# Kernel optimization log

Measured on AMD Instinct MI355X. Metric: run time of the kernel, lower is better.

Reference implementation:

```python
import jax, jax.numpy as jnp
import numpy as np
import math

N = 500_000
C_IN = 16
C_OUT = 64
H, W = 256, 256
PE_DIM = 32
BOUNDS = (-1.0, 1.0)
LN_EPS = 1e-5


def setup_inputs() -> dict:
    key = jax.random.key(0)
    ks = jax.random.split(key, 4)
    d_in = C_IN + 6 * PE_DIM  # 208
    pos = jax.random.uniform(ks[0], (N, 3), jnp.float32, minval=-1.0, maxval=1.0)
    features = jax.random.normal(ks[1], (N, C_IN), jnp.float32)
    W1 = jax.random.normal(ks[2], (d_in, C_OUT), jnp.float32) * (1.0 / math.sqrt(d_in))
    b1 = jnp.zeros((C_OUT,), jnp.float32)
    ln_g = jnp.ones((C_OUT,), jnp.float32)
    ln_b = jnp.zeros((C_OUT,), jnp.float32)
    W2 = jax.random.normal(ks[3], (C_OUT, C_OUT), jnp.float32) * (1.0 / math.sqrt(C_OUT))
    b2 = jnp.zeros((C_OUT,), jnp.float32)
    return {"pos": pos, "features": features, "W1": W1, "b1": b1,
            "ln_g": ln_g, "ln_b": ln_b, "W2": W2, "b2": b2,
            "axis1": 0, "axis2": 1}


def _pos_encode(pos):
    # sinusoidal encoding: per spatial dim, sin/cos at PE_DIM frequencies
    scale = BOUNDS[1] - BOUNDS[0]
    freq_bands = jnp.arange(PE_DIM, dtype=jnp.float32) / PE_DIM  # linspace(0,31,32)/32
    freqs = (pos / scale)[..., None] * (2.0 ** freq_bands) * math.pi  # [N,3,PE]
    # ordering per dim: sin_d, cos_d -> [N, 3*2*PE]
    enc = jnp.stack([jnp.sin(freqs), jnp.cos(freqs)], axis=2)  # [N,3,2,PE]
    return enc.reshape(pos.shape[0], 3 * 2 * PE_DIM)


def _layernorm(x, g, b):
    mu = jnp.mean(x, axis=-1, keepdims=True)
    var = jnp.var(x, axis=-1, keepdims=True)
    return (x - mu) * jax.lax.rsqrt(var + LN_EPS) * g + b


def reference(pos, features, W1, b1, ln_g, ln_b, W2, b2, axis1, axis2):
    # MLP on [features | pos_encoding]
    combined = jnp.concatenate([features, _pos_encode(pos)], axis=-1)  # [N,208]
    h = combined @ W1 + b1
    h = jax.nn.gelu(_layernorm(h, ln_g, ln_b), approximate=False)
    feat = h @ W2 + b2  # [N,C_OUT]

    # grid indices for the projected plane
    lo, hi = BOUNDS
    norm = jnp.clip((pos - lo) / (hi - lo), 0.0, 1.0)
    res = jnp.array([H, W], jnp.float32)
    i1 = jnp.clip(jnp.floor(norm[:, axis1] * res[0]), 0, H - 1).astype(jnp.int32)
    i2 = jnp.clip(jnp.floor(norm[:, axis2] * res[1]), 0, W - 1).astype(jnp.int32)
    flat = i1 * W + i2  # [N]

    # scatter-mean into grid
    sums = jax.ops.segment_sum(feat, flat, num_segments=H * W)  # [H*W, C]
    counts = jax.ops.segment_sum(jnp.ones((feat.shape[0],), jnp.float32), flat,
                                 num_segments=H * W)
    grid = sums / jnp.maximum(counts, 1.0)[:, None]  # [H*W, C]
    grid = grid.reshape(H, W, C_OUT).transpose(2, 0, 1)  # [C,H,W]
    return grid[None]  # [1,C,H,W]
```

## Files before the change

### kernel.cpp

```cpp
#include <hip/hip_runtime.h>
#include <math.h>

#define NPTS   500000
#define CIN    16
#define COUT   64
#define GRID_W 256
#define NCELL  65536

#define WS_HIST   0
#define WS_STARTS 262144
#define WS_CR     524288
#define WS_SORT   2621440
#define WS_WPK    4718592
#define WS_FEAT   4755456
#define WS_NEED   (WS_FEAT + (size_t)NPTS * COUT * 2)

#define PT_BLOCKS ((NPTS + 255) / 256)
#define MB_BLOCKS ((NPTS + 511) / 512)

#define W_HALFS   18432
#define W1_FRAGS  28

typedef _Float16 f16x8 __attribute__((ext_vector_type(8)));
typedef _Float16 f16x2 __attribute__((ext_vector_type(2)));
typedef float    f32x4 __attribute__((ext_vector_type(4)));

__device__ __forceinline__ f16x2 pk2(float a, float b) {
    auto r = __builtin_amdgcn_cvt_pkrtz(a, b);
    union { decltype(r) x; f16x2 y; } u; u.x = r;
    return u.y;
}

__device__ __forceinline__ float vsin(float x) {
    float r;
    asm("v_sin_f32 %0, %1" : "=v"(r) : "v"(x));
    return r;
}

__device__ __forceinline__ int cell_index(float v) {
    float nf = fminf(fmaxf((v + 1.0f) * 0.5f, 0.0f), 1.0f);
    int i = (int)floorf(nf * 256.0f);
    return i > 255 ? 255 : i;
}

__device__ __forceinline__ int flat_of(const float* pos, int p, int a1, int a2) {
    float pa1 = pos[p * 3 + a1];
    float pa2 = pos[p * 3 + a2];
    return cell_index(pa1) * GRID_W + cell_index(pa2);
}

__global__ void pack_hist_kernel(const float* __restrict__ W1,
                                 const float* __restrict__ W2,
                                 const float* __restrict__ pos,
                                 const int* __restrict__ ax1p,
                                 const int* __restrict__ ax2p,
                                 _Float16* __restrict__ wpk,
                                 unsigned int* __restrict__ hist,
                                 unsigned int* __restrict__ cr32)
{
    int i = blockIdx.x * 256 + threadIdx.x;
    if (i < W_HALFS) {
        int j = i & 7, lane = (i >> 3) & 63, f = i >> 9;
        int k  = ((f < W1_FRAGS) ? (f >> 2) : ((f - W1_FRAGS) >> 2)) * 32 + ((lane >> 4) << 3) + j;
        int ch = (f & 3) * 16 + (lane & 15);
        float v;
        if (f < W1_FRAGS) v = (k < 208) ? W1[k * 64 + ch] : 0.0f;
        else              v = W2[k * 64 + ch];
        wpk[i] = (_Float16)v;
    }
    if (i < NPTS) {
        int flat = flat_of(pos, i, ax1p[0], ax2p[0]);
        unsigned int old = atomicAdd(&hist[flat], 1u);
        if (cr32) cr32[i] = (unsigned int)flat | (old << 16);
    }
}

__global__ __launch_bounds__(1024)
void scan_fused_kernel(const unsigned int* __restrict__ hist,
                       unsigned int* __restrict__ starts)
{
    __shared__ unsigned int ssum[1024];
    const int t = threadIdx.x;
    const int base = t * 64;
    unsigned int s = 0;
    #pragma unroll
    for (int i = 0; i < 64; i += 4) {
        uint4 q = *(const uint4*)(hist + base + i);
        s += q.x + q.y + q.z + q.w;
    }
    ssum[t] = s;
    __syncthreads();
    for (int off = 1; off < 1024; off <<= 1) {
        unsigned int add = (t >= off) ? ssum[t - off] : 0u;
        __syncthreads();
        ssum[t] += add;
        __syncthreads();
    }
    unsigned int run = ssum[t] - s;
    #pragma unroll
    for (int i = 0; i < 64; i += 4) {
        uint4 q = *(const uint4*)(hist + base + i);
        starts[base + i + 0] = run; run += q.x;
        starts[base + i + 1] = run; run += q.y;
        starts[base + i + 2] = run; run += q.z;
        starts[base + i + 3] = run; run += q.w;
    }
}

__global__ void build_sorted_kernel(const unsigned int* __restrict__ cr32,
                                    const unsigned int* __restrict__ starts,
                                    int* __restrict__ sorted)
{
    int p = blockIdx.x * 256 + threadIdx.x;
    if (p >= NPTS) return;
    unsigned int cr = cr32[p];
    sorted[starts[cr & 0xFFFFu] + (cr >> 16)] = p;
}

__global__ __launch_bounds__(512, 4)
void mlp_mfma_kernel(const float* __restrict__ pos,
                     const float* __restrict__ feats,
                     const _Float16* __restrict__ wpk,
                     const float* __restrict__ b1,
                     const float* __restrict__ ln_g,
                     const float* __restrict__ ln_b,
                     const int*   __restrict__ ax1p,
                     const int*   __restrict__ ax2p,
                     _Float16* __restrict__ featbuf,
                     float* __restrict__ out,
                     int use_feat)
{
    __shared__ __align__(16) _Float16 WF[W_HALFS];
    __shared__ __align__(16) _Float16 PS[8 * 1024];

    {
        const uint4* src = (const uint4*)wpk;
        uint4* dst = (uint4*)WF;
        for (int i = threadIdx.x; i < W_HALFS / 8; i += 512) dst[i] = src[i];
    }

    const int lane = threadIdx.x & 63;
    const int wv   = threadIdx.x >> 6;
    const int g    = lane >> 4;
    const int n    = lane & 15;
    char* Pw = (char*)(PS + wv * 1024);
    const unsigned sw = (unsigned)((n & 7) << 4);

    const int wbase = blockIdx.x * 512 + wv * 64;

    const float base  = 0.25f * exp2f((float)((8 * g + 16) & 31) * 0.03125f);
    const float RSTEP = 1.02189714865411668f;

    __syncthreads();

    #pragma unroll 1
    for (int tp = 0; tp < 2; ++tp) {
        float px[2], py[2], pz[2];
        f16x8 fH[2];
        #pragma unroll
        for (int u = 0; u < 2; ++u) {
            const int st = wbase + (tp * 2 + u) * 16 + n;
            const int p  = (st < NPTS) ? st : 0;
            px[u] = pos[3 * p + 0];
            py[u] = pos[3 * p + 1];
            pz[u] = pos[3 * p + 2];
            if (g < 2) {
                const float4* fr = (const float4*)(feats + (size_t)p * CIN + g * 8);
                float4 fa = fr[0], fb = fr[1];
                union { f16x8 v; f16x2 h[4]; } Uf;
                Uf.h[0] = pk2(fa.x, fa.y); Uf.h[1] = pk2(fa.z, fa.w);
                Uf.h[2] = pk2(fb.x, fb.y); Uf.h[3] = pk2(fb.z, fb.w);
                fH[u] = Uf.v;
            }
        }

        f32x4 acc[2][4];
        #pragma unroll
        for (int u = 0; u < 2; ++u)
            #pragma unroll
            for (int c = 0; c < 4; ++c)
                acc[u][c] = (f32x4){0.0f, 0.0f, 0.0f, 0.0f};

        #pragma unroll
        for (int s = 0; s < 7; ++s) {
            f16x8 U[2];
            const int k0 = s * 32 + g * 8;
            if (s == 0 && g < 2) {
                U[0] = fH[0]; U[1] = fH[1];
            } else if (k0 >= 208) {
                union { f16x8 v; f16x2 h[4]; } Z;
                #pragma unroll
                for (int q = 0; q < 4; ++q) Z.h[q] = pk2(0.0f, 0.0f);
                U[0] = Z.v; U[1] = Z.v;
            } else {
                const int   e    = k0 - 16;
                const float off  = (e & 32) ? 0.25f : 0.0f;
                const float offc = (e & 32) ? (0.25f * (1.0f - RSTEP)) : 0.0f;
                #pragma unroll
                for (int u = 0; u < 2; ++u) {
                    const float pv = (e < 64) ? px[u] : ((e < 128) ? py[u] : pz[u]);
                    float a = fmaf(pv, base, off);
                    union { f16x8 v; f16x2 h[4]; } G;
                    #pragma unroll
                    for (int q = 0; q < 4; ++q) {
                        float v0 = vsin(a); a = fmaf(a, RSTEP, offc);
                        float v1 = vsin(a); a = fmaf(a, RSTEP, offc);
                        G.h[q] = pk2(v0, v1);
                    }
                    U[u] = G.v;
                }
            }
            #pragma unroll
            for (int c = 0; c < 4; ++c) {
                f16x8 af = ((const f16x8*)WF)[(s * 4 + c) * 64 + lane];
                acc[0][c] = __builtin_amdgcn_mfma_f32_16x16x32_f16(af, U[0], acc[0][c], 0, 0, 0);
                acc[1][c] = __builtin_amdgcn_mfma_f32_16x16x32_f16(af, U[1], acc[1][c], 0, 0, 0);
            }
        }

        #pragma unroll
        for (int u = 0; u < 2; ++u) {
            float s1 = 0.0f, s2 = 0.0f;
            #pragma unroll
            for (int c = 0; c < 4; ++c) {
                f32x4 b1q = *(const f32x4*)(b1 + 16 * c + 4 * g);
                #pragma unroll
                for (int r = 0; r < 4; ++r) {
                    float x = acc[u][c][r] + b1q[r];
                    acc[u][c][r] = x;
                    s1 += x; s2 += x * x;
                }
            }
            s1 += __shfl_xor(s1, 16); s2 += __shfl_xor(s2, 16);
            s1 += __shfl_xor(s1, 32); s2 += __shfl_xor(s2, 32);
            const float mu   = s1 * (1.0f / 64.0f);
            const float var  = s2 * (1.0f / 64.0f) - mu * mu;
            const float rstd = __builtin_amdgcn_rsqf(var + 1e-5f);

            #pragma unroll
            for (int c = 0; c < 4; ++c) {
                f32x4 gq = *(const f32x4*)(ln_g + 16 * c + 4 * g);
                f32x4 bq = *(const f32x4*)(ln_b + 16 * c + 4 * g);
                float gv[4];
                #pragma unroll
                for (int r = 0; r < 4; ++r) {
                    float x  = (acc[u][c][r] - mu) * rstd * gq[r] + bq[r];
                    float w  = x * (0.7978845608028654f + 0.0356774081363001f * x * x);
                    float e2 = __expf(w + w);
                    gv[r] = x * e2 * __builtin_amdgcn_rcpf(e2 + 1.0f);
                }
                union { f16x2 h[2]; uint2 u2; } W;
                W.h[0] = pk2(gv[0], gv[1]);
                W.h[1] = pk2(gv[2], gv[3]);
                *(uint2*)(Pw + n * 128 + (((unsigned)(32 * c + 8 * g)) ^ sw)) = W.u2;
            }

            f32x4 acc2[4];
            #pragma unroll
            for (int c = 0; c < 4; ++c) acc2[c] = (f32x4){0.0f, 0.0f, 0.0f, 0.0f};
            #pragma unroll
            for (int s = 0; s < 2; ++s) {
                f16x8 bf2 = *(const f16x8*)(Pw + n * 128 + (((unsigned)(64 * s + 16 * g)) ^ sw));
                #pragma unroll
                for (int c = 0; c < 4; ++c) {
                    f16x8 af = ((const f16x8*)WF)[(W1_FRAGS + s * 4 + c) * 64 + lane];
                    acc2[c] = __builtin_amdgcn_mfma_f32_16x16x32_f16(af, bf2, acc2[c], 0, 0, 0);
                }
            }

            if (use_feat) {
                const int gs = wbase + (tp * 2 + u) * 16 + n;
                if (gs < NPTS) {
                    _Float16* dstp = featbuf + (size_t)gs * COUT + 4 * g;
                    #pragma unroll
                    for (int c = 0; c < 4; ++c) {
                        union { f16x2 h[2]; uint2 u2; } W;
                        W.h[0] = pk2(acc2[c][0], acc2[c][1]);
                        W.h[1] = pk2(acc2[c][2], acc2[c][3]);
                        *(uint2*)(dstp + 16 * c) = W.u2;
                    }
                }
            } else {
                const int st = wbase + (tp * 2 + u) * 16 + n;
                if (st < NPTS) {
                    const int cellr = flat_of(pos, st, ax1p[0], ax2p[0]);
                    #pragma unroll
                    for (int c = 0; c < 4; ++c)
                        #pragma unroll
                        for (int r = 0; r < 4; ++r)
                            unsafeAtomicAdd(&out[(size_t)(16 * c + 4 * g + r) * NCELL + cellr],
                                            acc2[c][r]);
                }
            }
        }
    }
}

__global__ __launch_bounds__(1024)
void reduce_kernel(const _Float16* __restrict__ featbuf,
                   const int* __restrict__ sorted,
                   const unsigned int* __restrict__ starts,
                   const unsigned int* __restrict__ hist,
                   const float* __restrict__ b2,
                   float* __restrict__ out)
{
    __shared__ float R[16][66];
    const int lane  = threadIdx.x & 63;
    const int wv    = threadIdx.x >> 6;
    const int cbase = blockIdx.x * 16;
    const float b2v = b2[lane];

    const int cell = cbase + wv;
    const unsigned int s0  = starts[cell];
    const unsigned int cnt = hist[cell];

    float a0 = 0.0f, a1 = 0.0f, a2 = 0.0f, a3 = 0.0f;
    for (unsigned int k = 0; k < cnt; k += 4) {
        unsigned int i0 = s0 + k;
        unsigned int i1 = i0 + 1 < (unsigned)NPTS ? i0 + 1 : (unsigned)(NPTS - 1);
        unsigned int i2 = i0 + 2 < (unsigned)NPTS ? i0 + 2 : (unsigned)(NPTS - 1);
        unsigned int i3 = i0 + 3 < (unsigned)NPTS ? i0 + 3 : (unsigned)(NPTS - 1);
        int r0 = sorted[i0];
        int r1 = sorted[i1];
        int r2 = sorted[i2];
        int r3 = sorted[i3];
        float v0 = (float)featbuf[(size_t)r0 * COUT + lane];
        float v1 = (float)featbuf[(size_t)r1 * COUT + lane];
        float v2 = (float)featbuf[(size_t)r2 * COUT + lane];
        float v3 = (float)featbuf[(size_t)r3 * COUT + lane];
        a0 += v0;
        a1 += (k + 1 < cnt) ? v1 : 0.0f;
        a2 += (k + 2 < cnt) ? v2 : 0.0f;
        a3 += (k + 3 < cnt) ? v3 : 0.0f;
    }
    float m = (a0 + a1) + (a2 + a3);
    R[wv][lane] = m / fmaxf((float)cnt, 1.0f) + (cnt ? b2v : 0.0f);
    __syncthreads();

    const int ch = threadIdx.x >> 4;
    const int ci = threadIdx.x & 15;
    out[ch * NCELL + cbase + ci] = R[ci][ch];
}

__global__ void finalize_kernel(float* __restrict__ out,
                                const unsigned int* __restrict__ hist,
                                const float* __restrict__ b2)
{
    int t = blockIdx.x * 256 + threadIdx.x;
    int cell = t & (NCELL - 1);
    int ch   = t >> 16;
    float c  = (float)hist[cell];
    out[t] = out[t] / fmaxf(c, 1.0f) + ((c > 0.0f) ? b2[ch] : 0.0f);
}

extern "C" void kernel_launch(void* const* d_in, const int* in_sizes, int n_in,
                              void* d_out, int out_size, void* d_ws, size_t ws_size,
                              hipStream_t stream) {
    (void)in_sizes; (void)n_in; (void)out_size;
    const float* pos   = (const float*)d_in[0];
    const float* feats = (const float*)d_in[1];
    const float* W1    = (const float*)d_in[2];
    const float* b1    = (const float*)d_in[3];
    const float* ln_g  = (const float*)d_in[4];
    const float* ln_b  = (const float*)d_in[5];
    const float* W2    = (const float*)d_in[6];
    const float* b2    = (const float*)d_in[7];
    const int*   ax1   = (const int*)d_in[8];
    const int*   ax2   = (const int*)d_in[9];

    char* ws = (char*)d_ws;
    unsigned int* hist   = (unsigned int*)(ws + WS_HIST);
    unsigned int* starts = (unsigned int*)(ws + WS_STARTS);
    unsigned int* cr32   = (unsigned int*)(ws + WS_CR);
    int*          sorted = (int*)(ws + WS_SORT);
    _Float16*     wpk    = (_Float16*)(ws + WS_WPK);
    _Float16*     featbf = (_Float16*)(ws + WS_FEAT);

    float* out = (float*)d_out;
    const int use_feat = (ws_size >= WS_NEED) ? 1 : 0;

    hipMemsetAsync(hist, 0, NCELL * sizeof(unsigned int), stream);
    if (!use_feat)
        hipMemsetAsync(d_out, 0, (size_t)COUT * NCELL * sizeof(float), stream);

    pack_hist_kernel<<<PT_BLOCKS, 256, 0, stream>>>(
        W1, W2, pos, ax1, ax2, wpk, hist,
        use_feat ? cr32 : (unsigned int*)nullptr);
    if (use_feat) {
        scan_fused_kernel<<<1, 1024, 0, stream>>>(hist, starts);
        build_sorted_kernel<<<PT_BLOCKS, 256, 0, stream>>>(cr32, starts, sorted);
    }
    mlp_mfma_kernel<<<MB_BLOCKS, 512, 0, stream>>>(
        pos, feats, wpk, b1, ln_g, ln_b, ax1, ax2, featbf, out, use_feat);
    if (use_feat)
        reduce_kernel<<<NCELL / 16, 1024, 0, stream>>>(featbf, sorted, starts, hist, b2, out);
    else
        finalize_kernel<<<(COUT * NCELL) / 256, 256, 0, stream>>>(out, hist, b2);
}
```

Baseline: 226.9 us.

## Fuse histogram into MLP kernel, parallelize sin bases, vectorize cell reduction

Result: no change. 224.8 us (-0.9%).

```diff
diff --git a/kernel.cpp b/kernel.cpp
--- a/kernel.cpp
+++ b/kernel.cpp
@@ -43,36 +43,19 @@
     return i > 255 ? 255 : i;
 }
 
-__device__ __forceinline__ int flat_of(const float* pos, int p, int a1, int a2) {
-    float pa1 = pos[p * 3 + a1];
-    float pa2 = pos[p * 3 + a2];
-    return cell_index(pa1) * GRID_W + cell_index(pa2);
-}
-
-__global__ void pack_hist_kernel(const float* __restrict__ W1,
-                                 const float* __restrict__ W2,
-                                 const float* __restrict__ pos,
-                                 const int* __restrict__ ax1p,
-                                 const int* __restrict__ ax2p,
-                                 _Float16* __restrict__ wpk,
-                                 unsigned int* __restrict__ hist,
-                                 unsigned int* __restrict__ cr32)
+__global__ void pack_w_kernel(const float* __restrict__ W1,
+                              const float* __restrict__ W2,
+                              _Float16* __restrict__ wpk)
 {
     int i = blockIdx.x * 256 + threadIdx.x;
-    if (i < W_HALFS) {
-        int j = i & 7, lane = (i >> 3) & 63, f = i >> 9;
-        int k  = ((f < W1_FRAGS) ? (f >> 2) : ((f - W1_FRAGS) >> 2)) * 32 + ((lane >> 4) << 3) + j;
-        int ch = (f & 3) * 16 + (lane & 15);
-        float v;
-        if (f < W1_FRAGS) v = (k < 208) ? W1[k * 64 + ch] : 0.0f;
-        else              v = W2[k * 64 + ch];
-        wpk[i] = (_Float16)v;
-    }
-    if (i < NPTS) {
-        int flat = flat_of(pos, i, ax1p[0], ax2p[0]);
-        unsigned int old = atomicAdd(&hist[flat], 1u);
-        if (cr32) cr32[i] = (unsigned int)flat | (old << 16);
-    }
+    if (i >= W_HALFS) return;
+    int j = i & 7, lane = (i >> 3) & 63, f = i >> 9;
+    int k  = ((f < W1_FRAGS) ? (f >> 2) : ((f - W1_FRAGS) >> 2)) * 32 + ((lane >> 4) << 3) + j;
+    int ch = (f & 3) * 16 + (lane & 15);
+    float v;
+    if (f < W1_FRAGS) v = (k < 208) ? W1[k * 64 + ch] : 0.0f;
+    else              v = W2[k * 64 + ch];
+    wpk[i] = (_Float16)v;
 }
 
 __global__ __launch_bounds__(1024)
@@ -126,6 +109,8 @@
                      const float* __restrict__ ln_b,
                      const int*   __restrict__ ax1p,
                      const int*   __restrict__ ax2p,
+                     unsigned int* __restrict__ hist,
+                     unsigned int* __restrict__ cr32,
                      _Float16* __restrict__ featbuf,
                      float* __restrict__ out,
                      int use_feat)
@@ -147,9 +132,15 @@
     const unsigned sw = (unsigned)((n & 7) << 4);
 
     const int wbase = blockIdx.x * 512 + wv * 64;
-
-    const float base  = 0.25f * exp2f((float)((8 * g + 16) & 31) * 0.03125f);
-    const float RSTEP = 1.02189714865411668f;
+    const int a1 = ax1p[0], a2 = ax2p[0];
+
+    float bases[8];
+    {
+        const float f0 = (float)((8 * g + 16) & 31);
+        #pragma unroll
+        for (int q = 0; q < 8; ++q)
+            bases[q] = 0.25f * exp2f((f0 + (float)q) * 0.03125f);
+    }
 
     __syncthreads();
 
@@ -174,6 +165,20 @@
             }
         }
 
+        if (g == 0) {
+            #pragma unroll
+            for (int u = 0; u < 2; ++u) {
+                const int st = wbase + (tp * 2 + u) * 16 + n;
+                if (st < NPTS) {
+                    const float pa1 = (a1 == 0) ? px[u] : ((a1 == 1) ? py[u] : pz[u]);
+                    const float pa2 = (a2 == 0) ? px[u] : ((a2 == 1) ? py[u] : pz[u]);
+                    const int flat = cell_index(pa1) * GRID_W + cell_index(pa2);
+                    const unsigned int old = atomicAdd(&hist[flat], 1u);
+                    if (cr32) cr32[st] = (unsigned int)flat | (old << 16);
+                }
+            }
+        }
+
         f32x4 acc[2][4];
         #pragma unroll
         for (int u = 0; u < 2; ++u)
@@ -193,20 +198,19 @@
                 for (int q = 0; q < 4; ++q) Z.h[q] = pk2(0.0f, 0.0f);
                 U[0] = Z.v; U[1] = Z.v;
             } else {
-                const int   e    = k0 - 16;
-                const float off  = (e & 32) ? 0.25f : 0.0f;
-                const float offc = (e & 32) ? (0.25f * (1.0f - RSTEP)) : 0.0f;
+                const int   e   = k0 - 16;
+                const float off = (e & 32) ? 0.25f : 0.0f;
                 #pragma unroll
                 for (int u = 0; u < 2; ++u) {
                     const float pv = (e < 64) ? px[u] : ((e < 128) ? py[u] : pz[u]);
-                    float a = fmaf(pv, base, off);
+                    float sv[8];
+                    #pragma unroll
+                    for (int q = 0; q < 8; ++q)
+                        sv[q] = vsin(fmaf(pv, bases[q], off));
                     union { f16x8 v; f16x2 h[4]; } G;
                     #pragma unroll
-                    for (int q = 0; q < 4; ++q) {
-                        float v0 = vsin(a); a = fmaf(a, RSTEP, offc);
-                        float v1 = vsin(a); a = fmaf(a, RSTEP, offc);
-                        G.h[q] = pk2(v0, v1);
-                    }
+                    for (int q = 0; q < 4; ++q)
+                        G.h[q] = pk2(sv[2 * q], sv[2 * q + 1]);
                     U[u] = G.v;
                 }
             }
@@ -283,7 +287,9 @@
             } else {
                 const int st = wbase + (tp * 2 + u) * 16 + n;
                 if (st < NPTS) {
-                    const int cellr = flat_of(pos, st, ax1p[0], ax2p[0]);
+                    const float pa1 = (a1 == 0) ? px[u] : ((a1 == 1) ? py[u] : pz[u]);
+                    const float pa2 = (a2 == 0) ? px[u] : ((a2 == 1) ? py[u] : pz[u]);
+                    const int cellr = cell_index(pa1) * GRID_W + cell_index(pa2);
                     #pragma unroll
                     for (int c = 0; c < 4; ++c)
                         #pragma unroll
@@ -308,33 +314,44 @@
     const int lane  = threadIdx.x & 63;
     const int wv    = threadIdx.x >> 6;
     const int cbase = blockIdx.x * 16;
-    const float b2v = b2[lane];
+    const int cq    = lane & 7;
+    const int rsl   = lane >> 3;
 
     const int cell = cbase + wv;
     const unsigned int s0  = starts[cell];
     const unsigned int cnt = hist[cell];
 
-    float a0 = 0.0f, a1 = 0.0f, a2 = 0.0f, a3 = 0.0f;
-    for (unsigned int k = 0; k < cnt; k += 4) {
-        unsigned int i0 = s0 + k;
-        unsigned int i1 = i0 + 1 < (unsigned)NPTS ? i0 + 1 : (unsigned)(NPTS - 1);
-        unsigned int i2 = i0 + 2 < (unsigned)NPTS ? i0 + 2 : (unsigned)(NPTS - 1);
-        unsigned int i3 = i0 + 3 < (unsigned)NPTS ? i0 + 3 : (unsigned)(NPTS - 1);
-        int r0 = sorted[i0];
-        int r1 = sorted[i1];
-        int r2 = sorted[i2];
-        int r3 = sorted[i3];
-        float v0 = (float)featbuf[(size_t)r0 * COUT + lane];
-        float v1 = (float)featbuf[(size_t)r1 * COUT + lane];
-        float v2 = (float)featbuf[(size_t)r2 * COUT + lane];
-        float v3 = (float)featbuf[(size_t)r3 * COUT + lane];
-        a0 += v0;
-        a1 += (k + 1 < cnt) ? v1 : 0.0f;
-        a2 += (k + 2 < cnt) ? v2 : 0.0f;
-        a3 += (k + 3 < cnt) ? v3 : 0.0f;
-    }
-    float m = (a0 + a1) + (a2 + a3);
-    R[wv][lane] = m / fmaxf((float)cnt, 1.0f) + (cnt ? b2v : 0.0f);
+    float acc[8];
+    #pragma unroll
+    for (int j = 0; j < 8; ++j) acc[j] = 0.0f;
+
+    for (unsigned int k = 0; k < cnt; k += 8) {
+        const unsigned int kk = k + (unsigned int)rsl;
+        const bool ok = kk < cnt;
+        const int r = sorted[ok ? (s0 + kk) : s0];
+        union { uint4 u; f16x2 h[4]; } V;
+        V.u = *(const uint4*)(featbuf + (size_t)r * COUT + cq * 8);
+        #pragma unroll
+        for (int j = 0; j < 4; ++j) {
+            acc[2 * j]     += ok ? (float)V.h[j].x : 0.0f;
+            acc[2 * j + 1] += ok ? (float)V.h[j].y : 0.0f;
+        }
+    }
+    #pragma unroll
+    for (int m = 8; m <= 32; m <<= 1)
+        #pragma unroll
+        for (int j = 0; j < 8; ++j)
+            acc[j] += __shfl_xor(acc[j], m);
+
+    if (rsl == 0) {
+        const float inv = 1.0f / fmaxf((float)cnt, 1.0f);
+        float4 b2a = *(const float4*)(b2 + cq * 8);
+        float4 b2b = *(const float4*)(b2 + cq * 8 + 4);
+        const float bb[8] = {b2a.x, b2a.y, b2a.z, b2a.w, b2b.x, b2b.y, b2b.z, b2b.w};
+        #pragma unroll
+        for (int j = 0; j < 8; ++j)
+            R[wv][cq * 8 + j] = cnt ? (acc[j] * inv + bb[j]) : 0.0f;
+    }
     __syncthreads();
 
     const int ch = threadIdx.x >> 4;
@@ -383,17 +400,15 @@
     if (!use_feat)
         hipMemsetAsync(d_out, 0, (size_t)COUT * NCELL * sizeof(float), stream);
 
-    pack_hist_kernel<<<PT_BLOCKS, 256, 0, stream>>>(
-        W1, W2, pos, ax1, ax2, wpk, hist,
-        use_feat ? cr32 : (unsigned int*)nullptr);
+    pack_w_kernel<<<(W_HALFS + 255) / 256, 256, 0, stream>>>(W1, W2, wpk);
+    mlp_mfma_kernel<<<MB_BLOCKS, 512, 0, stream>>>(
+        pos, feats, wpk, b1, ln_g, ln_b, ax1, ax2, hist,
+        use_feat ? cr32 : (unsigned int*)nullptr, featbf, out, use_feat);
     if (use_feat) {
         scan_fused_kernel<<<1, 1024, 0, stream>>>(hist, starts);
         build_sorted_kernel<<<PT_BLOCKS, 256, 0, stream>>>(cr32, starts, sorted);
-    }
-    mlp_mfma_kernel<<<MB_BLOCKS, 512, 0, stream>>>(
-        pos, feats, wpk, b1, ln_g, ln_b, ax1, ax2, featbf, out, use_feat);
-    if (use_feat)
         reduce_kernel<<<NCELL / 16, 1024, 0, stream>>>(featbf, sorted, starts, hist, b2, out);
-    else
+    } else {
         finalize_kernel<<<(COUT * NCELL) / 256, 256, 0, stream>>>(out, hist, b2);
-}
+    }
+}
```
